# Optimization experiments

Measured on AMD Instinct MI355X. Metric: run time of the kernel, lower is better.

## Reference

```python
import jax, jax.numpy as jnp
import numpy as np

B = 524288
INPUT_SIZE = 128
HIDDEN_SIZE = 128


def setup_inputs() -> dict:
    key = jax.random.key(0)
    k1, k2, k3, k4, k5, k6 = jax.random.split(key, 6)
    input_ = jax.random.normal(k1, (B, INPUT_SIZE), dtype=jnp.float32)
    hidden = jax.random.normal(k2, (B, HIDDEN_SIZE), dtype=jnp.float32)
    weight_ih = jax.random.normal(k3, (INPUT_SIZE + HIDDEN_SIZE, HIDDEN_SIZE), dtype=jnp.float32)
    weight_hh = jax.random.normal(k4, (HIDDEN_SIZE + HIDDEN_SIZE, HIDDEN_SIZE), dtype=jnp.float32)
    bias_ih = jax.random.normal(k5, (HIDDEN_SIZE,), dtype=jnp.float32)
    bias_hh = jax.random.normal(k6, (HIDDEN_SIZE,), dtype=jnp.float32)
    return {
        "input_": input_,
        "hidden": hidden,
        "weight_ih": weight_ih,
        "weight_hh": weight_hh,
        "bias_ih": bias_ih,
        "bias_hh": bias_hh,
    }


def reference(input_, hidden, weight_ih, weight_hh, bias_ih, bias_hh):
    # combined = cat(input_, hidden); cell = sigmoid(combined @ W_ih + b_ih)
    # Avoid explicit concat copy by splitting the GEMM over the two blocks.
    w_i, w_h = weight_ih[:INPUT_SIZE], weight_ih[INPUT_SIZE:]
    cell = jax.nn.sigmoid(input_ @ w_i + hidden @ w_h + bias_ih)
    # hidden_out = sigmoid(cat(cell, hidden) @ W_hh + b_hh)
    w_c, w_h2 = weight_hh[:HIDDEN_SIZE], weight_hh[HIDDEN_SIZE:]
    hidden_out = jax.nn.sigmoid(cell @ w_c + hidden @ w_h2 + bias_hh)
    return hidden_out
```

## Files before the change

### kernel.cpp

```cpp
#include <hip/hip_runtime.h>


typedef __bf16 bf16x8 __attribute__((ext_vector_type(8)));
typedef float floatx4 __attribute__((ext_vector_type(4)));

__device__ __align__(16) __bf16 g_wpack[4][4096][8];

__global__ void pack_w(const float* __restrict__ wih, const float* __restrict__ whh) {
    int tid  = blockIdx.x * 256 + threadIdx.x;
    int m    = tid >> 12;
    int r    = tid & 4095;
    int lane = r & 63;
    int s    = (r >> 6) & 7;
    int t    = r >> 9;
    int quad = lane >> 4, lrow = lane & 15;
    const float* W = m ? whh : wih;
    int slot = (t * 8 + s) * 64 + lane;
#pragma unroll
    for (int j = 0; j < 8; ++j) {
        int k = s * 32 + quad * 8 + j;
        int n = t * 16 + lrow;
        float x = W[k * 128 + n];
        __bf16 h = (__bf16)x;
        __bf16 l = (__bf16)(x - (float)h);
        g_wpack[2 * m + 0][slot][j] = h;
        g_wpack[2 * m + 1][slot][j] = l;
    }
}

__device__ __forceinline__ float sigmoid_fast(float x) {
    return __builtin_amdgcn_rcpf(1.0f + __expf(-x));
}

__global__ __launch_bounds__(256, 2) void lstm_fused(
        const float* __restrict__ input_,
        const float* __restrict__ hidden,
        const float* __restrict__ bias_ih,
        const float* __restrict__ bias_hh,
        float* __restrict__ out) {
    __shared__ __align__(16) float cell[4][32][132];

    const int wave = threadIdx.x >> 6;
    const int lane = threadIdx.x & 63;
    const int quad = lane >> 4;
    const int lrow = lane & 15;
    const long rowBase = (long)blockIdx.x * 128 + wave * 32;

    float bih[8], bhh[8];
#pragma unroll
    for (int t = 0; t < 8; ++t) {
        bih[t] = bias_ih[t * 16 + lrow];
        bhh[t] = bias_hh[t * 16 + lrow];
    }

    floatx4 acc[2][8];
#pragma unroll
    for (int mt = 0; mt < 2; ++mt)
#pragma unroll
        for (int t = 0; t < 8; ++t)
#pragma unroll
            for (int r = 0; r < 4; ++r)
                acc[mt][t][r] = 0.0f;

    bf16x8 hh_hi[2][4], hh_lo[2][4];

#pragma unroll
    for (int s = 0; s < 8; ++s) {
        bf16x8 a_hi[2], a_lo[2];
#pragma unroll
        for (int mt = 0; mt < 2; ++mt) {
            const float* src = (s < 4) ? input_ : hidden;
            const float* p = src + (rowBase + mt * 16 + lrow) * 128 + (s & 3) * 32 + quad * 8;
            floatx4 f0 = *(const floatx4*)p;
            floatx4 f1 = *(const floatx4*)(p + 4);
#pragma unroll
            for (int j = 0; j < 4; ++j) {
                __bf16 h0 = (__bf16)f0[j];
                a_hi[mt][j] = h0;
                a_lo[mt][j] = (__bf16)(f0[j] - (float)h0);
                __bf16 h1 = (__bf16)f1[j];
                a_hi[mt][4 + j] = h1;
                a_lo[mt][4 + j] = (__bf16)(f1[j] - (float)h1);
            }
            if (s >= 4) { hh_hi[mt][s - 4] = a_hi[mt]; hh_lo[mt][s - 4] = a_lo[mt]; }
        }
#pragma unroll
        for (int t = 0; t < 8; ++t) {
            bf16x8 bh = *(const bf16x8*)&g_wpack[0][(t * 8 + s) * 64 + lane][0];
            bf16x8 bl = *(const bf16x8*)&g_wpack[1][(t * 8 + s) * 64 + lane][0];
#pragma unroll
            for (int mt = 0; mt < 2; ++mt) {
                acc[mt][t] = __builtin_amdgcn_mfma_f32_16x16x32_bf16(a_hi[mt], bh, acc[mt][t], 0, 0, 0);
                acc[mt][t] = __builtin_amdgcn_mfma_f32_16x16x32_bf16(a_lo[mt], bh, acc[mt][t], 0, 0, 0);
                acc[mt][t] = __builtin_amdgcn_mfma_f32_16x16x32_bf16(a_hi[mt], bl, acc[mt][t], 0, 0, 0);
            }
        }
    }

#pragma unroll
    for (int mt = 0; mt < 2; ++mt)
#pragma unroll
        for (int t = 0; t < 8; ++t)
#pragma unroll
            for (int r = 0; r < 4; ++r) {
                float x = acc[mt][t][r] + bih[t];
                cell[wave][mt * 16 + quad * 4 + r][t * 16 + lrow] = sigmoid_fast(x);
                acc[mt][t][r] = 0.0f;
            }
    __syncthreads();

#pragma unroll
    for (int s = 0; s < 8; ++s) {
        bf16x8 a_hi[2], a_lo[2];
#pragma unroll
        for (int mt = 0; mt < 2; ++mt) {
            if (s < 4) {
                const float* p = &cell[wave][mt * 16 + lrow][s * 32 + quad * 8];
                floatx4 f0 = *(const floatx4*)p;
                floatx4 f1 = *(const floatx4*)(p + 4);
#pragma unroll
                for (int j = 0; j < 4; ++j) {
                    __bf16 h0 = (__bf16)f0[j];
                    a_hi[mt][j] = h0;
                    a_lo[mt][j] = (__bf16)(f0[j] - (float)h0);
                    __bf16 h1 = (__bf16)f1[j];
                    a_hi[mt][4 + j] = h1;
                    a_lo[mt][4 + j] = (__bf16)(f1[j] - (float)h1);
                }
            } else {
                a_hi[mt] = hh_hi[mt][s - 4];
                a_lo[mt] = hh_lo[mt][s - 4];
            }
        }
#pragma unroll
        for (int t = 0; t < 8; ++t) {
            bf16x8 bh = *(const bf16x8*)&g_wpack[2][(t * 8 + s) * 64 + lane][0];
            bf16x8 bl = *(const bf16x8*)&g_wpack[3][(t * 8 + s) * 64 + lane][0];
#pragma unroll
            for (int mt = 0; mt < 2; ++mt) {
                acc[mt][t] = __builtin_amdgcn_mfma_f32_16x16x32_bf16(a_hi[mt], bh, acc[mt][t], 0, 0, 0);
                acc[mt][t] = __builtin_amdgcn_mfma_f32_16x16x32_bf16(a_lo[mt], bh, acc[mt][t], 0, 0, 0);
                acc[mt][t] = __builtin_amdgcn_mfma_f32_16x16x32_bf16(a_hi[mt], bl, acc[mt][t], 0, 0, 0);
            }
        }
    }

#pragma unroll
    for (int mt = 0; mt < 2; ++mt)
#pragma unroll
        for (int t = 0; t < 8; ++t)
#pragma unroll
            for (int r = 0; r < 4; ++r) {
                float x = acc[mt][t][r] + bhh[t];
                out[(rowBase + mt * 16 + quad * 4 + r) * 128 + t * 16 + lrow] = sigmoid_fast(x);
            }
}

extern "C" void kernel_launch(void* const* d_in, const int* in_sizes, int n_in,
                              void* d_out, int out_size, void* d_ws, size_t ws_size,
                              hipStream_t stream) {
    const float* input_ = (const float*)d_in[0];
    const float* hidden = (const float*)d_in[1];
    const float* wih    = (const float*)d_in[2];
    const float* whh    = (const float*)d_in[3];
    const float* bih    = (const float*)d_in[4];
    const float* bhh    = (const float*)d_in[5];
    float* out = (float*)d_out;

    pack_w<<<32, 256, 0, stream>>>(wih, whh);
    lstm_fused<<<4096, 256, 0, stream>>>(input_, hidden, bih, bhh, out);
}
```

Measured before the change: 818.7 us.

## Shrink per-wave tile to 16 rows, raise occupancy, replace barrier with waitcnt

Each wave now computes 16 rows instead of 32, which halves the accumulator and A-fragment register state. Launch bounds rise to 4 blocks per SM and the grid doubles. The aim is more waves resident to hide global-load latency. The block-wide __syncthreads is replaced by an lgkmcnt wait, since each wave reads only its own LDS slice, and bias loads move to the epilogue. The cost is that every weight fragment loaded from global/L2 now feeds half as many MFMAs, so weight traffic per output row doubles.

```diff
diff --git a/kernel.cpp b/kernel.cpp
--- a/kernel.cpp
+++ b/kernel.cpp
@@ -32,128 +32,107 @@
     return __builtin_amdgcn_rcpf(1.0f + __expf(-x));
 }
 
-__global__ __launch_bounds__(256, 2) void lstm_fused(
+__global__ __launch_bounds__(256, 4) void lstm_fused(
         const float* __restrict__ input_,
         const float* __restrict__ hidden,
         const float* __restrict__ bias_ih,
         const float* __restrict__ bias_hh,
         float* __restrict__ out) {
-    __shared__ __align__(16) float cell[4][32][132];
+    __shared__ __align__(16) float cell[4][16][132];
 
     const int wave = threadIdx.x >> 6;
     const int lane = threadIdx.x & 63;
     const int quad = lane >> 4;
     const int lrow = lane & 15;
-    const long rowBase = (long)blockIdx.x * 128 + wave * 32;
+    const long rowBase = (long)blockIdx.x * 64 + wave * 16;
 
-    float bih[8], bhh[8];
+    floatx4 acc[8];
 #pragma unroll
-    for (int t = 0; t < 8; ++t) {
-        bih[t] = bias_ih[t * 16 + lrow];
-        bhh[t] = bias_hh[t * 16 + lrow];
-    }
+    for (int t = 0; t < 8; ++t)
+#pragma unroll
+        for (int r = 0; r < 4; ++r)
+            acc[t][r] = 0.0f;
 
-    floatx4 acc[2][8];
-#pragma unroll
-    for (int mt = 0; mt < 2; ++mt)
-#pragma unroll
-        for (int t = 0; t < 8; ++t)
-#pragma unroll
-            for (int r = 0; r < 4; ++r)
-                acc[mt][t][r] = 0.0f;
-
-    bf16x8 hh_hi[2][4], hh_lo[2][4];
+    bf16x8 hh_hi[4], hh_lo[4];
 
 #pragma unroll
     for (int s = 0; s < 8; ++s) {
-        bf16x8 a_hi[2], a_lo[2];
+        const float* src = (s < 4) ? input_ : hidden;
+        const float* p = src + (rowBase + lrow) * 128 + (s & 3) * 32 + quad * 8;
+        floatx4 f0 = *(const floatx4*)p;
+        floatx4 f1 = *(const floatx4*)(p + 4);
+        bf16x8 a_hi, a_lo;
 #pragma unroll
-        for (int mt = 0; mt < 2; ++mt) {
-            const float* src = (s < 4) ? input_ : hidden;
-            const float* p = src + (rowBase + mt * 16 + lrow) * 128 + (s & 3) * 32 + quad * 8;
+        for (int j = 0; j < 4; ++j) {
+            __bf16 h0 = (__bf16)f0[j];
+            a_hi[j] = h0;
+            a_lo[j] = (__bf16)(f0[j] - (float)h0);
+            __bf16 h1 = (__bf16)f1[j];
+            a_hi[4 + j] = h1;
+            a_lo[4 + j] = (__bf16)(f1[j] - (float)h1);
+        }
+        if (s >= 4) { hh_hi[s - 4] = a_hi; hh_lo[s - 4] = a_lo; }
+#pragma unroll
+        for (int t = 0; t < 8; ++t) {
+            bf16x8 bh = *(const bf16x8*)&g_wpack[0][(t * 8 + s) * 64 + lane][0];
+            bf16x8 bl = *(const bf16x8*)&g_wpack[1][(t * 8 + s) * 64 + lane][0];
+            acc[t] = __builtin_amdgcn_mfma_f32_16x16x32_bf16(a_hi, bh, acc[t], 0, 0, 0);
+            acc[t] = __builtin_amdgcn_mfma_f32_16x16x32_bf16(a_lo, bh, acc[t], 0, 0, 0);
+            acc[t] = __builtin_amdgcn_mfma_f32_16x16x32_bf16(a_hi, bl, acc[t], 0, 0, 0);
+        }
+    }
+
+#pragma unroll
+    for (int t = 0; t < 8; ++t) {
+        float bi = bias_ih[t * 16 + lrow];
+#pragma unroll
+        for (int r = 0; r < 4; ++r) {
+            float x = acc[t][r] + bi;
+            cell[wave][quad * 4 + r][t * 16 + lrow] = sigmoid_fast(x);
+            acc[t][r] = 0.0f;
+        }
+    }
+    asm volatile("s_waitcnt lgkmcnt(0)" ::: "memory");
+
+#pragma unroll
+    for (int s = 0; s < 8; ++s) {
+        bf16x8 a_hi, a_lo;
+        if (s < 4) {
+            const float* p = &cell[wave][lrow][s * 32 + quad * 8];
             floatx4 f0 = *(const floatx4*)p;
             floatx4 f1 = *(const floatx4*)(p + 4);
 #pragma unroll
             for (int j = 0; j < 4; ++j) {
                 __bf16 h0 = (__bf16)f0[j];
-                a_hi[mt][j] = h0;
-                a_lo[mt][j] = (__bf16)(f0[j] - (float)h0);
+                a_hi[j] = h0;
+                a_lo[j] = (__bf16)(f0[j] - (float)h0);
                 __bf16 h1 = (__bf16)f1[j];
-                a_hi[mt][4 + j] = h1;
-                a_lo[mt][4 + j] = (__bf16)(f1[j] - (float)h1);
+                a_hi[4 + j] = h1;
+                a_lo[4 + j] = (__bf16)(f1[j] - (float)h1);
             }
-            if (s >= 4) { hh_hi[mt][s - 4] = a_hi[mt]; hh_lo[mt][s - 4] = a_lo[mt]; }
-        }
-#pragma unroll
-        for (int t = 0; t < 8; ++t) {
-            bf16x8 bh = *(const bf16x8*)&g_wpack[0][(t * 8 + s) * 64 + lane][0];
-            bf16x8 bl = *(const bf16x8*)&g_wpack[1][(t * 8 + s) * 64 + lane][0];
-#pragma unroll
-            for (int mt = 0; mt < 2; ++mt) {
-                acc[mt][t] = __builtin_amdgcn_mfma_f32_16x16x32_bf16(a_hi[mt], bh, acc[mt][t], 0, 0, 0);
-                acc[mt][t] = __builtin_amdgcn_mfma_f32_16x16x32_bf16(a_lo[mt], bh, acc[mt][t], 0, 0, 0);
-                acc[mt][t] = __builtin_amdgcn_mfma_f32_16x16x32_bf16(a_hi[mt], bl, acc[mt][t], 0, 0, 0);
-            }
-        }
-    }
-
-#pragma unroll
-    for (int mt = 0; mt < 2; ++mt)
-#pragma unroll
-        for (int t = 0; t < 8; ++t)
-#pragma unroll
-            for (int r = 0; r < 4; ++r) {
-                float x = acc[mt][t][r] + bih[t];
-                cell[wave][mt * 16 + quad * 4 + r][t * 16 + lrow] = sigmoid_fast(x);
-                acc[mt][t][r] = 0.0f;
-            }
-    __syncthreads();
-
-#pragma unroll
-    for (int s = 0; s < 8; ++s) {
-        bf16x8 a_hi[2], a_lo[2];
-#pragma unroll
-        for (int mt = 0; mt < 2; ++mt) {
-            if (s < 4) {
-                const float* p = &cell[wave][mt * 16 + lrow][s * 32 + quad * 8];
-                floatx4 f0 = *(const floatx4*)p;
-                floatx4 f1 = *(const floatx4*)(p + 4);
-#pragma unroll
-                for (int j = 0; j < 4; ++j) {
-                    __bf16 h0 = (__bf16)f0[j];
-                    a_hi[mt][j] = h0;
-                    a_lo[mt][j] = (__bf16)(f0[j] - (float)h0);
-                    __bf16 h1 = (__bf16)f1[j];
-                    a_hi[mt][4 + j] = h1;
-                    a_lo[mt][4 + j] = (__bf16)(f1[j] - (float)h1);
-                }
-            } else {
-                a_hi[mt] = hh_hi[mt][s - 4];
-                a_lo[mt] = hh_lo[mt][s - 4];
-            }
+        } else {
+            a_hi = hh_hi[s - 4];
+            a_lo = hh_lo[s - 4];
         }
 #pragma unroll
         for (int t = 0; t < 8; ++t) {
             bf16x8 bh = *(const bf16x8*)&g_wpack[2][(t * 8 + s) * 64 + lane][0];
             bf16x8 bl = *(const bf16x8*)&g_wpack[3][(t * 8 + s) * 64 + lane][0];
-#pragma unroll
-            for (int mt = 0; mt < 2; ++mt) {
-                acc[mt][t] = __builtin_amdgcn_mfma_f32_16x16x32_bf16(a_hi[mt], bh, acc[mt][t], 0, 0, 0);
-                acc[mt][t] = __builtin_amdgcn_mfma_f32_16x16x32_bf16(a_lo[mt], bh, acc[mt][t], 0, 0, 0);
-                acc[mt][t] = __builtin_amdgcn_mfma_f32_16x16x32_bf16(a_hi[mt], bl, acc[mt][t], 0, 0, 0);
-            }
+            acc[t] = __builtin_amdgcn_mfma_f32_16x16x32_bf16(a_hi, bh, acc[t], 0, 0, 0);
+            acc[t] = __builtin_amdgcn_mfma_f32_16x16x32_bf16(a_lo, bh, acc[t], 0, 0, 0);
+            acc[t] = __builtin_amdgcn_mfma_f32_16x16x32_bf16(a_hi, bl, acc[t], 0, 0, 0);
         }
     }
 
 #pragma unroll
-    for (int mt = 0; mt < 2; ++mt)
+    for (int t = 0; t < 8; ++t) {
+        float bh_ = bias_hh[t * 16 + lrow];
 #pragma unroll
-        for (int t = 0; t < 8; ++t)
-#pragma unroll
-            for (int r = 0; r < 4; ++r) {
-                float x = acc[mt][t][r] + bhh[t];
-                out[(rowBase + mt * 16 + quad * 4 + r) * 128 + t * 16 + lrow] = sigmoid_fast(x);
-            }
+        for (int r = 0; r < 4; ++r) {
+            float x = acc[t][r] + bh_;
+            out[(rowBase + quad * 4 + r) * 128 + t * 16 + lrow] = sigmoid_fast(x);
+        }
+    }
 }
 
 extern "C" void kernel_launch(void* const* d_in, const int* in_sizes, int n_in,
@@ -168,5 +147,5 @@
     float* out = (float*)d_out;
 
     pack_w<<<32, 256, 0, stream>>>(wih, whh);
-    lstm_fused<<<4096, 256, 0, stream>>>(input_, hidden, bih, bhh, out);
+    lstm_fused<<<8192, 256, 0, stream>>>(input_, hidden, bih, bhh, out);
 }
```

Result: slower. 929.4 us (+13.5%).
